# Optimization experiments

Measured on AMD Instinct MI355X. Metric: run time of the kernel, lower is better.

Reference implementation:

```python
import jax, jax.numpy as jnp
import numpy as np
import math

B, S, D, H = 2, 2048, 1024, 16
HD = D // H


def _rms_norm(x, scale):
    # norm over (seq, d_model) jointly per batch element, as in the source
    b, s, d = x.shape
    ff_rms = jnp.sqrt(jnp.sum(x * x, axis=(1, 2))) * (s * d) ** -0.5  # (B,)
    return scale[None, :s, :] * (x / ff_rms[:, None, None])


def _rope(x):
    # faithful to _generate_rope_matrix: theta = 10000^(-2*(i-1)/D) (note i-1)
    b, s, d = x.shape
    i = jnp.arange(d // 2, dtype=jnp.float32)
    theta = 10000.0 ** (-2.0 * (i - 1.0) / d)            # (D/2,)
    ang = jnp.arange(s, dtype=jnp.float32)[:, None] * theta[None, :]  # (S, D/2)
    cos, sin = jnp.cos(ang), jnp.sin(ang)
    xp = x.reshape(b, s, d // 2, 2)
    xe, xo = xp[..., 0], xp[..., 1]
    # out = x @ R[pos]; R block [[cos,-sin],[sin,cos]] per pair
    oe = xe * cos + xo * sin
    oo = -xe * sin + xo * cos
    return jnp.stack([oe, oo], axis=-1).reshape(b, s, d)


def _alibi_mask(s, h):
    r = jnp.arange(s)
    dist = r[:, None] - r[None, :]                        # row j - col i
    base = jnp.where(dist < 0, -jnp.inf, -dist.astype(jnp.float32))  # (S,S)
    ratio = 2.0 ** (-8.0 / h)
    slopes = ratio ** jnp.arange(1, h + 1, dtype=jnp.float32)        # (H,)
    return base[None, :, :] * slopes[:, None, None]       # (H,S,S)


def setup_inputs() -> dict:
    key = jax.random.key(0)
    ks = jax.random.split(key, 9)
    p = lambda k, shp: jax.random.normal(k, shp, jnp.float32) * 0.02
    return {
        "x": jax.random.normal(ks[0], (B, S, D), jnp.float32),
        "Wq": p(ks[1], (D, D)), "Wk": p(ks[2], (D, D)),
        "Wv": p(ks[3], (D, D)), "Wo": p(ks[4], (D, D)),
        "scale1": jnp.ones((S, D), jnp.float32),
        "scale2": jnp.ones((S, D), jnp.float32),
        "W1": p(ks[5], (D, D)), "b1": jnp.zeros((D,), jnp.float32),
        "Wg": p(ks[6], (D, D)), "bg": jnp.zeros((D,), jnp.float32),
        "Wl": p(ks[7], (D, D)), "bl": jnp.zeros((D,), jnp.float32),
        "beta": jnp.ones((1,), jnp.float32),
    }


def reference(x, Wq, Wk, Wv, Wo, scale1, scale2, W1, b1, Wg, bg, Wl, bl, beta):
    b, s, d = x.shape
    # --- attention sublayer ---
    h = _rms_norm(x, scale1)
    q = _rope(h @ Wq)
    k = _rope(h @ Wk)
    v = _rope(h @ Wv)
    qh = q.reshape(b, s, H, HD).transpose(0, 2, 1, 3)  # (B,H,S,HD)
    kh = k.reshape(b, s, H, HD).transpose(0, 2, 1, 3)
    vh = v.reshape(b, s, H, HD).transpose(0, 2, 1, 3)
    mask = _alibi_mask(s, H)                           # (H,S,S)
    scores = jnp.einsum("bhqd,bhkd->bhqk", qh, kh) * (1.0 / math.sqrt(HD))
    probs = jax.nn.softmax(scores + mask[None], axis=-1)
    o = jnp.einsum("bhqk,bhkd->bhqd", probs, vh)
    o = o.transpose(0, 2, 1, 3).reshape(b, s, d)
    x_res_1 = x + o @ Wo
    # --- FFN sublayer: Linear -> SwiGLU ---
    h2 = _rms_norm(x_res_1, scale2) @ W1 + b1
    g = h2 @ Wg + bg
    swish_gate = g * jax.nn.sigmoid(beta * g)
    ffn = swish_gate * (h2 @ Wl + bl)
    return x_res_1 + ffn
```

## Files before the change

### kernel.cpp

```cpp
#include <hip/hip_runtime.h>
#include <hip/hip_bf16.h>

typedef __attribute__((ext_vector_type(8))) short bf16x8;
typedef __attribute__((ext_vector_type(4))) float f32x4;
typedef __attribute__((ext_vector_type(4))) int int4v;

#define DEV static __device__ __forceinline__

DEV float b2f(unsigned short u) { union { unsigned int i; float f; } c; c.i = ((unsigned int)u) << 16; return c.f; }
DEV unsigned short f2b(float f) {
  __hip_bfloat16 h = __float2bfloat16(f);
  unsigned short u; __builtin_memcpy(&u, &h, 2); return u;
}

DEV void gload16(const void* g, void* l) {
  __builtin_amdgcn_global_load_lds(
      (const __attribute__((address_space(1))) unsigned int*)(g),
      (__attribute__((address_space(3))) unsigned int*)(l), 16, 0, 0);
}

__global__ __launch_bounds__(256) void k_transpose_w(const float* __restrict__ W,
                                                     unsigned short* __restrict__ Wt) {
  __shared__ float tile[32][33];
  const int tx = threadIdx.x & 31, ty = threadIdx.x >> 5;
  const int c0 = blockIdx.x * 32, r0 = blockIdx.y * 32;
#pragma unroll
  for (int i = 0; i < 4; ++i)
    tile[ty + i * 8][tx] = W[(size_t)(r0 + ty + i * 8) * 1024 + c0 + tx];
  __syncthreads();
#pragma unroll
  for (int i = 0; i < 4; ++i)
    Wt[(size_t)(c0 + ty + i * 8) * 1024 + r0 + tx] = f2b(tile[tx][ty + i * 8]);
}

__global__ __launch_bounds__(256) void k_reduce_sq(const float* __restrict__ x,
                                                   float* __restrict__ sums) {
  const int b = blockIdx.y;
  const float4* xb = (const float4*)(x + (size_t)b * 2097152);
  float s = 0.f;
  for (int i = blockIdx.x * 256 + threadIdx.x; i < 524288; i += 256 * gridDim.x) {
    float4 v = xb[i];
    s += v.x * v.x + v.y * v.y + v.z * v.z + v.w * v.w;
  }
  __shared__ float red[256];
  red[threadIdx.x] = s;
  __syncthreads();
  for (int st = 128; st > 0; st >>= 1) {
    if (threadIdx.x < st) red[threadIdx.x] += red[threadIdx.x + st];
    __syncthreads();
  }
  if (threadIdx.x == 0) atomicAdd(&sums[b], red[0]);
}

__global__ __launch_bounds__(256) void k_rmsnorm(const float* __restrict__ x,
                                                 const float* __restrict__ scale,
                                                 const float* __restrict__ sums,
                                                 unsigned short* __restrict__ out) {
  const int idx = blockIdx.x * 256 + threadIdx.x;
  const int e = idx * 4;
  const int m = e >> 10, d = e & 1023;
  const int b = m >> 11, s = m & 2047;
  const float inv = rsqrtf(sums[b] * (1.0f / 2097152.0f));
  float4 xv = *(const float4*)(x + (size_t)e);
  float4 sv = *(const float4*)(scale + (size_t)s * 1024 + d);
  ushort4 o;
  o.x = f2b(xv.x * sv.x * inv); o.y = f2b(xv.y * sv.y * inv);
  o.z = f2b(xv.z * sv.z * inv); o.w = f2b(xv.w * sv.w * inv);
  *(ushort4*)(out + e) = o;
}

template <int EPI, int NREP>
__global__ __launch_bounds__(256) void k_gemm(const unsigned short* __restrict__ A,
                                              const unsigned short* __restrict__ Bt,
                                              void* __restrict__ Cout,
                                              const float* __restrict__ aux,
                                              const int N,
                                              float* __restrict__ ss) {
  constexpr int BN = NREP * 32;
  __shared__ short As[128 * 64];
  __shared__ short Bs[BN * 64];
  const int tid = threadIdx.x;
  const int w = tid >> 6, l = tid & 63;
  const int brow = blockIdx.y * 128, bcol = blockIdx.x * BN;
  const int wr = (w >> 1) * 64, wc = (w & 1) * (NREP * 16);
  const int lr = l >> 3, lg = l & 7;
  f32x4 acc[4][NREP] = {};
  const short* Ag = (const short*)A;
  const short* Bg = (const short*)Bt;
  for (int k0 = 0; k0 < 1024; k0 += 64) {
    __syncthreads();
#pragma unroll
    for (int p = 0; p < 4; ++p) {
      const int row = p * 32 + w * 8 + lr;
      gload16(Ag + (size_t)(brow + row) * 1024 + k0 + lg * 8,
              (char*)As + (size_t)(p * 32 + w * 8) * 128);
    }
#pragma unroll
    for (int p = 0; p < NREP; ++p) {
      const int row = p * 32 + w * 8 + lr;
      gload16(Bg + (size_t)(bcol + row) * 1024 + k0 + lg * 8,
              (char*)Bs + (size_t)(p * 32 + w * 8) * 128);
    }
    __syncthreads();
#pragma unroll
    for (int kk = 0; kk < 2; ++kk) {
      const int g0 = kk * 4 + (l >> 4);
      bf16x8 af[4], bfr[NREP];
#pragma unroll
      for (int m = 0; m < 4; ++m)
        af[m] = *(const bf16x8*)(As + (wr + m * 16 + (l & 15)) * 64 + g0 * 8);
#pragma unroll
      for (int n = 0; n < NREP; ++n)
        bfr[n] = *(const bf16x8*)(Bs + (wc + n * 16 + (l & 15)) * 64 + g0 * 8);
#pragma unroll
      for (int m = 0; m < 4; ++m)
#pragma unroll
        for (int n = 0; n < NREP; ++n)
          acc[m][n] = __builtin_amdgcn_mfma_f32_16x16x32_bf16(af[m], bfr[n], acc[m][n], 0, 0, 0);
    }
  }
  const int rr = (l >> 4) * 4, cc = l & 15;
  float sq = 0.f;
#pragma unroll
  for (int m = 0; m < 4; ++m)
#pragma unroll
    for (int n = 0; n < NREP; ++n) {
      const int col = bcol + wc + n * 16 + cc;
#pragma unroll
      for (int j = 0; j < 4; ++j) {
        const int row = brow + wr + m * 16 + rr + j;
        float v = acc[m][n][j];
        if (EPI == 0) {
          ((unsigned short*)Cout)[(size_t)row * N + col] = f2b(v);
        } else if (EPI == 1) {
          const float v2 = aux[(size_t)row * N + col] + v;
          ((float*)Cout)[(size_t)row * N + col] = v2;
          sq += v2 * v2;
        } else {
          ((unsigned short*)Cout)[(size_t)row * N + col] = f2b(v + aux[col]);
        }
      }
    }
  if (EPI == 1) {
#pragma unroll
    for (int off = 1; off < 64; off <<= 1) sq += __shfl_xor(sq, off);
    if (l == 0) atomicAdd(&ss[brow >> 11], sq);
  }
}

__global__ __launch_bounds__(256) void k_rope(unsigned int* __restrict__ qkv32) {
  const int p = blockIdx.x * 256 + threadIdx.x;
  const int m = p / 1536;
  const int pc = p - m * 1536;
  const int s = m & 2047;
  const int i = pc & 511;
  const float theta = expf(-((float)i - 1.0f) * 0.017988946039016f);
  const float ang = (float)s * theta;
  float sn, cs;
  sincosf(ang, &sn, &cs);
  unsigned int v = qkv32[p];
  float xe = b2f((unsigned short)(v & 0xffffu));
  float xo = b2f((unsigned short)(v >> 16));
  float oe = xe * cs + xo * sn;
  float oo = -xe * sn + xo * cs;
  qkv32[p] = (unsigned int)f2b(oe) | ((unsigned int)f2b(oo) << 16);
}

__global__ __launch_bounds__(256) void k_transpose_v(const unsigned short* __restrict__ qkv,
                                                     unsigned short* __restrict__ vt) {
  __shared__ unsigned short tile[32][33];
  const int tx = threadIdx.x & 31, ty = threadIdx.x >> 5;
  const int bh = blockIdx.z;
  const int b = bh >> 4, h = bh & 15;
  const int d0 = blockIdx.x * 32, s0 = blockIdx.y * 32;
#pragma unroll
  for (int i = 0; i < 4; ++i)
    tile[ty + i * 8][tx] = qkv[(size_t)(b * 2048 + s0 + ty + i * 8) * 3072 + 2048 + h * 64 + d0 + tx];
  __syncthreads();
#pragma unroll
  for (int i = 0; i < 4; ++i)
    vt[((size_t)bh * 64 + d0 + ty + i * 8) * 2048 + s0 + tx] = tile[tx][ty + i * 8];
}

__global__ __launch_bounds__(256) void k_attn(const unsigned short* __restrict__ qkv,
                                              const unsigned short* __restrict__ vt,
                                              unsigned short* __restrict__ o) {
  __shared__ short Ks[2][4096];
  __shared__ short Vs[2][4096];
  __shared__ short Ps[4][1280];
  const int h = blockIdx.y, b = blockIdx.z;
  const int qtA = blockIdx.x, qtB = 31 - qtA;
  const int tid = threadIdx.x, w = tid >> 6, l = tid & 63;
  const short* qg = (const short*)qkv;
  bf16x8 aqA0, aqA1, aqB0, aqB1;
  {
    const int rowA = qtA * 64 + w * 16 + (l & 15);
    const short* baseA = qg + (size_t)(b * 2048 + rowA) * 3072 + h * 64 + (l >> 4) * 8;
    aqA0 = *(const bf16x8*)(baseA);
    aqA1 = *(const bf16x8*)(baseA + 32);
    const int rowB = qtB * 64 + w * 16 + (l & 15);
    const short* baseB = qg + (size_t)(b * 2048 + rowB) * 3072 + h * 64 + (l >> 4) * 8;
    aqB0 = *(const bf16x8*)(baseB);
    aqB1 = *(const bf16x8*)(baseB + 32);
  }
  const float slope = exp2f(-0.5f * (float)(h + 1));
  f32x4 oacc[4] = {};
  float mrun[4] = {-1e30f, -1e30f, -1e30f, -1e30f};
  float lrun[4] = {0.f, 0.f, 0.f, 0.f};
  short* Pw = &Ps[w][0];
  const int c0 = tid, c1 = tid + 256;
  const int r0 = c0 >> 3, g0c = c0 & 7;
  const int r1 = c1 >> 3, g1c = c1 & 7;
  const int s0 = r0 * 64 + ((g0c ^ (r0 & 7)) * 8);
  const int s1 = r1 * 64 + ((g1c ^ (r1 & 7)) * 8);
  const short* kbase = qg + (size_t)(b * 2048) * 3072 + 1024 + h * 64;
  const short* vbase = (const short*)vt + (size_t)(b * 16 + h) * 64 * 2048;
  const int nA = qtA + 1;
  const int nt = 33;
  *(int4v*)(&Ks[0][s0]) = *(const int4v*)(kbase + (size_t)r0 * 3072 + g0c * 8);
  *(int4v*)(&Ks[0][s1]) = *(const int4v*)(kbase + (size_t)r1 * 3072 + g1c * 8);
  *(int4v*)(&Vs[0][s0]) = *(const int4v*)(vbase + (size_t)r0 * 2048 + g0c * 8);
  *(int4v*)(&Vs[0][s1]) = *(const int4v*)(vbase + (size_t)r1 * 2048 + g1c * 8);
  __syncthreads();

  auto writeout = [&](int q0w) {
    const int rr = (l >> 4) * 4, cc = l & 15;
#pragma unroll
    for (int n = 0; n < 4; ++n)
#pragma unroll
      for (int j = 0; j < 4; ++j) {
        const int row = q0w + w * 16 + rr + j;
        const int col = h * 64 + n * 16 + cc;
        o[(size_t)(b * 2048 + row) * 1024 + col] = f2b(oacc[n][j] / lrun[j]);
      }
  };

  int cur = 0;
  for (int i = 0; i < nt; ++i) {
    int4v kr0, kr1, vr0, vr1;
    const int inx = i + 1;
    const bool havenext = (inx < nt);
    if (havenext) {
      const int kvn = (inx < nA) ? inx : (inx - nA);
      const size_t k0n = (size_t)kvn * 64;
      kr0 = *(const int4v*)(kbase + (k0n + r0) * 3072 + g0c * 8);
      kr1 = *(const int4v*)(kbase + (k0n + r1) * 3072 + g1c * 8);
      vr0 = *(const int4v*)(vbase + (size_t)r0 * 2048 + k0n + g0c * 8);
      vr1 = *(const int4v*)(vbase + (size_t)r1 * 2048 + k0n + g1c * 8);
    }
    const bool phaseB = (i >= nA);
    const int kvt = phaseB ? (i - nA) : i;
    const int kv0 = kvt * 64;
    const int q0 = (phaseB ? qtB : qtA) * 64;
    const int qw = q0 + w * 16;
    bf16x8 aq0, aq1;
    if (phaseB) { aq0 = aqB0; aq1 = aqB1; } else { aq0 = aqA0; aq1 = aqA1; }
    const short* Ksc = &Ks[cur][0];
    const short* Vsc = &Vs[cur][0];
    f32x4 sacc[4] = {};
    __builtin_amdgcn_s_setprio(1);
#pragma unroll
    for (int kk = 0; kk < 2; ++kk) {
      const int g0r = kk * 4 + (l >> 4);
      const bf16x8 aqk = kk ? aq1 : aq0;
#pragma unroll
      for (int n = 0; n < 4; ++n) {
        const int col = n * 16 + (l & 15);
        bf16x8 bk = *(const bf16x8*)(Ksc + col * 64 + ((g0r ^ (col & 7)) * 8));
        sacc[n] = __builtin_amdgcn_mfma_f32_16x16x32_bf16(aqk, bk, sacc[n], 0, 0, 0);
      }
    }
    __builtin_amdgcn_s_setprio(0);
    float pv[4][4];
    float rm[4] = {-3e30f, -3e30f, -3e30f, -3e30f};
#pragma unroll
    for (int n = 0; n < 4; ++n) {
      const int kvg = kv0 + n * 16 + (l & 15);
#pragma unroll
      for (int j = 0; j < 4; ++j) {
        const int qrow = qw + (l >> 4) * 4 + j;
        float v;
        if (kvg <= qrow) v = sacc[n][j] * 0.125f + slope * (float)(kvg - qrow);
        else v = -1e30f;
        pv[n][j] = v;
        rm[j] = fmaxf(rm[j], v);
      }
    }
#pragma unroll
    for (int j = 0; j < 4; ++j) {
      rm[j] = fmaxf(rm[j], __shfl_xor(rm[j], 1));
      rm[j] = fmaxf(rm[j], __shfl_xor(rm[j], 2));
      rm[j] = fmaxf(rm[j], __shfl_xor(rm[j], 4));
      rm[j] = fmaxf(rm[j], __shfl_xor(rm[j], 8));
    }
    float corr[4], rs[4];
#pragma unroll
    for (int j = 0; j < 4; ++j) {
      const float mn = fmaxf(mrun[j], rm[j]);
      corr[j] = __expf(mrun[j] - mn);
      mrun[j] = mn;
      rs[j] = 0.f;
    }
#pragma unroll
    for (int n = 0; n < 4; ++n)
#pragma unroll
      for (int j = 0; j < 4; ++j) {
        const float e = __expf(pv[n][j] - mrun[j]);
        pv[n][j] = e;
        rs[j] += e;
      }
#pragma unroll
    for (int j = 0; j < 4; ++j) {
      rs[j] += __shfl_xor(rs[j], 1);
      rs[j] += __shfl_xor(rs[j], 2);
      rs[j] += __shfl_xor(rs[j], 4);
      rs[j] += __shfl_xor(rs[j], 8);
      lrun[j] = lrun[j] * corr[j] + rs[j];
    }
#pragma unroll
    for (int n = 0; n < 4; ++n)
#pragma unroll
      for (int j = 0; j < 4; ++j) oacc[n][j] *= corr[j];
#pragma unroll
    for (int n = 0; n < 4; ++n)
#pragma unroll
      for (int j = 0; j < 4; ++j)
        Pw[((l >> 4) * 4 + j) * 80 + n * 16 + (l & 15)] = (short)f2b(pv[n][j]);
    __builtin_amdgcn_s_setprio(1);
#pragma unroll
    for (int kk2 = 0; kk2 < 2; ++kk2) {
      bf16x8 pf = *(const bf16x8*)(Pw + (l & 15) * 80 + kk2 * 32 + (l >> 4) * 8);
#pragma unroll
      for (int n = 0; n < 4; ++n) {
        const int dr = n * 16 + (l & 15);
        bf16x8 vf = *(const bf16x8*)(Vsc + dr * 64 + (((kk2 * 4 + (l >> 4)) ^ (dr & 7)) * 8));
        oacc[n] = __builtin_amdgcn_mfma_f32_16x16x32_bf16(pf, vf, oacc[n], 0, 0, 0);
      }
    }
    __builtin_amdgcn_s_setprio(0);
    if (i == nA - 1) {
      writeout(qtA * 64);
#pragma unroll
      for (int n = 0; n < 4; ++n) oacc[n] = f32x4{0.f, 0.f, 0.f, 0.f};
#pragma unroll
      for (int j = 0; j < 4; ++j) { mrun[j] = -1e30f; lrun[j] = 0.f; }
    }
    if (havenext) {
      const int nxt = cur ^ 1;
      *(int4v*)(&Ks[nxt][s0]) = kr0;
      *(int4v*)(&Ks[nxt][s1]) = kr1;
      *(int4v*)(&Vs[nxt][s0]) = vr0;
      *(int4v*)(&Vs[nxt][s1]) = vr1;
    }
    __syncthreads();
    cur ^= 1;
  }
  writeout(qtB * 64);
}

__global__ __launch_bounds__(256) void k_final(const float* __restrict__ x1,
                                               const unsigned short* __restrict__ gl,
                                               const float* __restrict__ beta,
                                               float* __restrict__ out) {
  const int idx = blockIdx.x * 256 + threadIdx.x;
  const int e = idx * 4;
  const int m = e >> 10, d = e & 1023;
  const float bt = beta[0];
  ushort4 gu = *(const ushort4*)(gl + (size_t)m * 2048 + d);
  ushort4 lu = *(const ushort4*)(gl + (size_t)m * 2048 + 1024 + d);
  float4 xv = *(const float4*)(x1 + e);
  float g0 = b2f(gu.x), g1 = b2f(gu.y), g2 = b2f(gu.z), g3 = b2f(gu.w);
  float l0 = b2f(lu.x), l1 = b2f(lu.y), l2 = b2f(lu.z), l3 = b2f(lu.w);
  float4 r;
  r.x = xv.x + g0 / (1.f + __expf(-bt * g0)) * l0;
  r.y = xv.y + g1 / (1.f + __expf(-bt * g1)) * l1;
  r.z = xv.z + g2 / (1.f + __expf(-bt * g2)) * l2;
  r.w = xv.w + g3 / (1.f + __expf(-bt * g3)) * l3;
  *(float4*)(out + e) = r;
}

extern "C" void kernel_launch(void* const* d_in, const int* in_sizes, int n_in,
                              void* d_out, int out_size, void* d_ws, size_t ws_size,
                              hipStream_t stream) {
  (void)in_sizes; (void)n_in; (void)out_size; (void)ws_size;
  const float* x      = (const float*)d_in[0];
  const float* Wq     = (const float*)d_in[1];
  const float* Wk     = (const float*)d_in[2];
  const float* Wv     = (const float*)d_in[3];
  const float* Wo     = (const float*)d_in[4];
  const float* scale1 = (const float*)d_in[5];
  const float* scale2 = (const float*)d_in[6];
  const float* W1     = (const float*)d_in[7];
  const float* b1     = (const float*)d_in[8];
  const float* Wg     = (const float*)d_in[9];
  const float* bg     = (const float*)d_in[10];
  const float* Wl     = (const float*)d_in[11];
  const float* bl     = (const float*)d_in[12];
  const float* beta   = (const float*)d_in[13];
  float* out = (float*)d_out;

  char* ws = (char*)d_ws;
  float* sums         = (float*)ws;
  float* bgl          = (float*)(ws + 256);
  unsigned short* WT  = (unsigned short*)(ws + 16384);
  unsigned short* h   = (unsigned short*)(ws + 16384 + 6291456);
  unsigned short* qkv = (unsigned short*)((char*)h + 8388608);
  unsigned short* vt  = (unsigned short*)((char*)qkv + 25165824);
  unsigned short* ob  = (unsigned short*)((char*)vt + 8388608);
  float* x1           = (float*)((char*)ob + 8388608);
  unsigned short* t1  = qkv;
  unsigned short* gl  = qkv + 4194304;

  hipMemsetAsync(sums, 0, 256, stream);

  k_transpose_w<<<dim3(32, 32), 256, 0, stream>>>(Wq, WT);
  k_transpose_w<<<dim3(32, 32), 256, 0, stream>>>(Wk, WT + 1048576);
  k_transpose_w<<<dim3(32, 32), 256, 0, stream>>>(Wv, WT + 2097152);
  k_reduce_sq<<<dim3(256, 2), 256, 0, stream>>>(x, sums);
  k_rmsnorm<<<4096, 256, 0, stream>>>(x, scale1, sums, h);
  k_gemm<0, 4><<<dim3(24, 32), 256, 0, stream>>>(h, WT, (void*)qkv, nullptr, 3072, nullptr);
  k_rope<<<24576, 256, 0, stream>>>((unsigned int*)qkv);
  k_transpose_v<<<dim3(2, 64, 32), 256, 0, stream>>>(qkv, vt);
  k_attn<<<dim3(16, 16, 2), 256, 0, stream>>>(qkv, vt, ob);
  k_transpose_w<<<dim3(32, 32), 256, 0, stream>>>(Wo, WT);
  k_gemm<1, 2><<<dim3(16, 32), 256, 0, stream>>>(ob, WT, (void*)x1, x, 1024, sums + 2);

  k_rmsnorm<<<4096, 256, 0, stream>>>(x1, scale2, sums + 2, h);
  k_transpose_w<<<dim3(32, 32), 256, 0, stream>>>(W1, WT);
  k_gemm<2, 2><<<dim3(16, 32), 256, 0, stream>>>(h, WT, (void*)t1, b1, 1024, nullptr);
  k_transpose_w<<<dim3(32, 32), 256, 0, stream>>>(Wg, WT);
  k_transpose_w<<<dim3(32, 32), 256, 0, stream>>>(Wl, WT + 1048576);
  hipMemcpyAsync(bgl, bg, 4096, hipMemcpyDeviceToDevice, stream);
  hipMemcpyAsync(bgl + 1024, bl, 4096, hipMemcpyDeviceToDevice, stream);
  k_gemm<2, 4><<<dim3(16, 32), 256, 0, stream>>>(t1, WT, (void*)gl, bgl, 2048, nullptr);
  k_final<<<4096, 256, 0, stream>>>(x1, gl, beta, out);
}
```

Before: 395.2 us.

## Fuse weight transposes, SwiGLU epilogue, interleave attention tiles, vectorize RoPE

Merges the seven weight-transpose launches into one kernel and drops the bias memcpys. Fuses the SwiGLU, bias and residual into the final GEMM's epilogue, so the gate/linear intermediate and the separate final kernel go away. Restructures attention to process both query tiles of a pair in the same KV loop, computing row sums with an MFMA against a ones vector and using exp2 with folded constants. Remaps attention blocks for XCD locality and vectorizes RoPE with fast sincos, trading some precision for fewer instructions.

```diff
diff --git a/kernel.cpp b/kernel.cpp
--- a/kernel.cpp
+++ b/kernel.cpp
@@ -19,9 +19,22 @@
       (__attribute__((address_space(3))) unsigned int*)(l), 16, 0, 0);
 }
 
-__global__ __launch_bounds__(256) void k_transpose_w(const float* __restrict__ W,
-                                                     unsigned short* __restrict__ Wt) {
+__global__ __launch_bounds__(256) void k_transpose_w7(const float* __restrict__ Wq,
+                                                      const float* __restrict__ Wk,
+                                                      const float* __restrict__ Wv,
+                                                      const float* __restrict__ Wo,
+                                                      const float* __restrict__ W1,
+                                                      const float* __restrict__ Wg,
+                                                      const float* __restrict__ Wl,
+                                                      unsigned short* __restrict__ WT) {
   __shared__ float tile[32][33];
+  const float* W;
+  switch (blockIdx.z) {
+    case 0: W = Wq; break; case 1: W = Wk; break; case 2: W = Wv; break;
+    case 3: W = Wo; break; case 4: W = W1; break; case 5: W = Wg; break;
+    default: W = Wl; break;
+  }
+  unsigned short* dst = WT + (size_t)blockIdx.z * 1048576;
   const int tx = threadIdx.x & 31, ty = threadIdx.x >> 5;
   const int c0 = blockIdx.x * 32, r0 = blockIdx.y * 32;
 #pragma unroll
@@ -30,7 +43,7 @@
   __syncthreads();
 #pragma unroll
   for (int i = 0; i < 4; ++i)
-    Wt[(size_t)(c0 + ty + i * 8) * 1024 + r0 + tx] = f2b(tile[tx][ty + i * 8]);
+    dst[(size_t)(c0 + ty + i * 8) * 1024 + r0 + tx] = f2b(tile[tx][ty + i * 8]);
 }
 
 __global__ __launch_bounds__(256) void k_reduce_sq(const float* __restrict__ x,
@@ -74,6 +87,9 @@
                                               const unsigned short* __restrict__ Bt,
                                               void* __restrict__ Cout,
                                               const float* __restrict__ aux,
+                                              const float* __restrict__ aux2,
+                                              const float* __restrict__ x1p,
+                                              const float* __restrict__ betap,
                                               const int N,
                                               float* __restrict__ ss) {
   constexpr int BN = NREP * 32;
@@ -81,8 +97,10 @@
   __shared__ short Bs[BN * 64];
   const int tid = threadIdx.x;
   const int w = tid >> 6, l = tid & 63;
-  const int brow = blockIdx.y * 128, bcol = blockIdx.x * BN;
-  const int wr = (w >> 1) * 64, wc = (w & 1) * (NREP * 16);
+  const int brow = blockIdx.y * 128;
+  const int bcol = blockIdx.x * (EPI == 4 ? 64 : BN);
+  const int wr = (w >> 1) * 64;
+  const int wc = (EPI == 4) ? (w & 1) * 32 : (w & 1) * (NREP * 16);
   const int lr = l >> 3, lg = l & 7;
   f32x4 acc[4][NREP] = {};
   const short* Ag = (const short*)A;
@@ -98,7 +116,12 @@
 #pragma unroll
     for (int p = 0; p < NREP; ++p) {
       const int row = p * 32 + w * 8 + lr;
-      gload16(Bg + (size_t)(bcol + row) * 1024 + k0 + lg * 8,
+      size_t goff;
+      if (EPI == 4 && p >= 2)
+        goff = (size_t)1048576 + (size_t)(bcol + row - 64) * 1024;
+      else
+        goff = (size_t)(bcol + row) * 1024;
+      gload16(Bg + goff + k0 + lg * 8,
               (char*)Bs + (size_t)(p * 32 + w * 8) * 128);
     }
     __syncthreads();
@@ -110,8 +133,12 @@
       for (int m = 0; m < 4; ++m)
         af[m] = *(const bf16x8*)(As + (wr + m * 16 + (l & 15)) * 64 + g0 * 8);
 #pragma unroll
-      for (int n = 0; n < NREP; ++n)
-        bfr[n] = *(const bf16x8*)(Bs + (wc + n * 16 + (l & 15)) * 64 + g0 * 8);
+      for (int n = 0; n < NREP; ++n) {
+        int bsrow;
+        if (EPI == 4) bsrow = (n < 2) ? (wc + n * 16 + (l & 15)) : (64 + wc + (n - 2) * 16 + (l & 15));
+        else bsrow = wc + n * 16 + (l & 15);
+        bfr[n] = *(const bf16x8*)(Bs + bsrow * 64 + g0 * 8);
+      }
 #pragma unroll
       for (int m = 0; m < 4; ++m)
 #pragma unroll
@@ -120,6 +147,24 @@
     }
   }
   const int rr = (l >> 4) * 4, cc = l & 15;
+  if (EPI == 4) {
+    const float bt = betap[0];
+#pragma unroll
+    for (int m = 0; m < 4; ++m)
+#pragma unroll
+      for (int nn = 0; nn < 2; ++nn) {
+        const int col = bcol + wc + nn * 16 + cc;
+#pragma unroll
+        for (int j = 0; j < 4; ++j) {
+          const int row = brow + wr + m * 16 + rr + j;
+          const float gv = acc[m][nn][j] + aux[col];
+          const float lv = acc[m][nn + 2][j] + aux2[col];
+          const float sw = gv / (1.f + __expf(-bt * gv));
+          ((float*)Cout)[(size_t)row * 1024 + col] = x1p[(size_t)row * 1024 + col] + sw * lv;
+        }
+      }
+    return;
+  }
   float sq = 0.f;
 #pragma unroll
   for (int m = 0; m < 4; ++m)
@@ -149,21 +194,27 @@
 }
 
 __global__ __launch_bounds__(256) void k_rope(unsigned int* __restrict__ qkv32) {
-  const int p = blockIdx.x * 256 + threadIdx.x;
-  const int m = p / 1536;
-  const int pc = p - m * 1536;
+  const int t = blockIdx.x * 256 + threadIdx.x;
+  const int p0 = t * 4;
+  const int m = p0 / 1536;
+  const int pc0 = p0 - m * 1536;
   const int s = m & 2047;
-  const int i = pc & 511;
-  const float theta = expf(-((float)i - 1.0f) * 0.017988946039016f);
-  const float ang = (float)s * theta;
-  float sn, cs;
-  sincosf(ang, &sn, &cs);
-  unsigned int v = qkv32[p];
-  float xe = b2f((unsigned short)(v & 0xffffu));
-  float xo = b2f((unsigned short)(v >> 16));
-  float oe = xe * cs + xo * sn;
-  float oo = -xe * sn + xo * cs;
-  qkv32[p] = (unsigned int)f2b(oe) | ((unsigned int)f2b(oo) << 16);
+  int4v v = *(const int4v*)(qkv32 + p0);
+#pragma unroll
+  for (int z = 0; z < 4; ++z) {
+    const int i = (pc0 + z) & 511;
+    const float theta = exp2f(-((float)i - 1.0f) * 0.0259525627f);
+    const float ang = (float)s * theta;
+    float sn, cs;
+    __sincosf(ang, &sn, &cs);
+    const unsigned int u = (unsigned int)v[z];
+    const float xe = b2f((unsigned short)(u & 0xffffu));
+    const float xo = b2f((unsigned short)(u >> 16));
+    const float oe = xe * cs + xo * sn;
+    const float oo = -xe * sn + xo * cs;
+    v[z] = (int)((unsigned int)f2b(oe) | ((unsigned int)f2b(oo) << 16));
+  }
+  *(int4v*)(qkv32 + p0) = v;
 }
 
 __global__ __launch_bounds__(256) void k_transpose_v(const unsigned short* __restrict__ qkv,
@@ -187,27 +238,37 @@
                                               unsigned short* __restrict__ o) {
   __shared__ short Ks[2][4096];
   __shared__ short Vs[2][4096];
-  __shared__ short Ps[4][1280];
-  const int h = blockIdx.y, b = blockIdx.z;
-  const int qtA = blockIdx.x, qtB = 31 - qtA;
+  __shared__ short Ps[8][1280];
+  const int id = blockIdx.x;
+  const int xcd = id & 7, q = id >> 3;
+  const int p = q & 15, g = (q >> 4) * 8 + xcd;
+  const int h = g & 15, b = g >> 4;
+  const int qtA = p, qtB = 31 - p;
+  const int nA = qtA + 1, nB = qtB + 1;
   const int tid = threadIdx.x, w = tid >> 6, l = tid & 63;
+  const int cc = l & 15, hi = l >> 4;
+  const int qwA = qtA * 64 + w * 16, qwB = qtB * 64 + w * 16;
   const short* qg = (const short*)qkv;
   bf16x8 aqA0, aqA1, aqB0, aqB1;
   {
-    const int rowA = qtA * 64 + w * 16 + (l & 15);
-    const short* baseA = qg + (size_t)(b * 2048 + rowA) * 3072 + h * 64 + (l >> 4) * 8;
-    aqA0 = *(const bf16x8*)(baseA);
+    const short* baseA = qg + (size_t)(b * 2048 + qwA + cc) * 3072 + h * 64 + hi * 8;
+    aqA0 = *(const bf16x8*)baseA;
     aqA1 = *(const bf16x8*)(baseA + 32);
-    const int rowB = qtB * 64 + w * 16 + (l & 15);
-    const short* baseB = qg + (size_t)(b * 2048 + rowB) * 3072 + h * 64 + (l >> 4) * 8;
-    aqB0 = *(const bf16x8*)(baseB);
+    const short* baseB = qg + (size_t)(b * 2048 + qwB + cc) * 3072 + h * 64 + hi * 8;
+    aqB0 = *(const bf16x8*)baseB;
     aqB1 = *(const bf16x8*)(baseB + 32);
   }
-  const float slope = exp2f(-0.5f * (float)(h + 1));
-  f32x4 oacc[4] = {};
-  float mrun[4] = {-1e30f, -1e30f, -1e30f, -1e30f};
-  float lrun[4] = {0.f, 0.f, 0.f, 0.f};
-  short* Pw = &Ps[w][0];
+  const float slope2 = exp2f(-0.5f * (float)(h + 1)) * 1.44269504f;
+  const float C1 = 0.125f * 1.44269504f;
+  bf16x8 onesf;
+#pragma unroll
+  for (int z = 0; z < 8; ++z) onesf[z] = (short)0x3F80;
+  f32x4 oaccA[4] = {}, oaccB[4] = {};
+  f32x4 rsA = {}, rsB = {};
+  float mA[4] = {-1e30f, -1e30f, -1e30f, -1e30f};
+  float mB[4] = {-1e30f, -1e30f, -1e30f, -1e30f};
+  short* PwA = &Ps[w][0];
+  short* PwB = &Ps[w + 4][0];
   const int c0 = tid, c1 = tid + 256;
   const int r0 = c0 >> 3, g0c = c0 & 7;
   const int r1 = c1 >> 3, g1c = c1 & 7;
@@ -215,136 +276,118 @@
   const int s1 = r1 * 64 + ((g1c ^ (r1 & 7)) * 8);
   const short* kbase = qg + (size_t)(b * 2048) * 3072 + 1024 + h * 64;
   const short* vbase = (const short*)vt + (size_t)(b * 16 + h) * 64 * 2048;
-  const int nA = qtA + 1;
-  const int nt = 33;
   *(int4v*)(&Ks[0][s0]) = *(const int4v*)(kbase + (size_t)r0 * 3072 + g0c * 8);
   *(int4v*)(&Ks[0][s1]) = *(const int4v*)(kbase + (size_t)r1 * 3072 + g1c * 8);
   *(int4v*)(&Vs[0][s0]) = *(const int4v*)(vbase + (size_t)r0 * 2048 + g0c * 8);
   *(int4v*)(&Vs[0][s1]) = *(const int4v*)(vbase + (size_t)r1 * 2048 + g1c * 8);
   __syncthreads();
 
-  auto writeout = [&](int q0w) {
-    const int rr = (l >> 4) * 4, cc = l & 15;
+  auto sm_pv = [&](f32x4 (&sacc)[4], f32x4 (&oacc)[4], f32x4& rs, float (&mr)[4],
+                   short* Pw, const int qw, const bool domask, const int kv0,
+                   const short* Vsc) {
+    float alib[4];
+#pragma unroll
+    for (int n = 0; n < 4; ++n) alib[n] = slope2 * (float)(kv0 + n * 16 + cc);
+    float sc[4][4], rm4[4];
+#pragma unroll
+    for (int j = 0; j < 4; ++j) rm4[j] = -3e30f;
 #pragma unroll
     for (int n = 0; n < 4; ++n)
 #pragma unroll
       for (int j = 0; j < 4; ++j) {
-        const int row = q0w + w * 16 + rr + j;
-        const int col = h * 64 + n * 16 + cc;
-        o[(size_t)(b * 2048 + row) * 1024 + col] = f2b(oacc[n][j] / lrun[j]);
-      }
+        float v = fmaf(sacc[n][j], C1, alib[n]);
+        if (domask) {
+          const int kvg = kv0 + n * 16 + cc;
+          const int qrow = qw + hi * 4 + j;
+          v = (kvg <= qrow) ? v : -1e30f;
+        }
+        sc[n][j] = v;
+        rm4[j] = fmaxf(rm4[j], v);
+      }
+#pragma unroll
+    for (int j = 0; j < 4; ++j) {
+      rm4[j] = fmaxf(rm4[j], __shfl_xor(rm4[j], 1));
+      rm4[j] = fmaxf(rm4[j], __shfl_xor(rm4[j], 2));
+      rm4[j] = fmaxf(rm4[j], __shfl_xor(rm4[j], 4));
+      rm4[j] = fmaxf(rm4[j], __shfl_xor(rm4[j], 8));
+    }
+    float corr[4];
+#pragma unroll
+    for (int j = 0; j < 4; ++j) {
+      const float mn = fmaxf(mr[j], rm4[j]);
+      corr[j] = exp2f(mr[j] - mn);
+      mr[j] = mn;
+    }
+#pragma unroll
+    for (int n = 0; n < 4; ++n)
+#pragma unroll
+      for (int j = 0; j < 4; ++j)
+        Pw[(hi * 4 + j) * 80 + n * 16 + cc] = (short)f2b(exp2f(sc[n][j] - mr[j]));
+#pragma unroll
+    for (int n = 0; n < 4; ++n)
+#pragma unroll
+      for (int j = 0; j < 4; ++j) oacc[n][j] *= corr[j];
+#pragma unroll
+    for (int j = 0; j < 4; ++j) rs[j] *= corr[j];
+    __builtin_amdgcn_s_setprio(1);
+#pragma unroll
+    for (int kk2 = 0; kk2 < 2; ++kk2) {
+      bf16x8 pf = *(const bf16x8*)(Pw + cc * 80 + kk2 * 32 + hi * 8);
+      rs = __builtin_amdgcn_mfma_f32_16x16x32_bf16(pf, onesf, rs, 0, 0, 0);
+#pragma unroll
+      for (int n = 0; n < 4; ++n) {
+        const int dr = n * 16 + cc;
+        bf16x8 vf = *(const bf16x8*)(Vsc + dr * 64 + (((kk2 * 4 + hi) ^ (dr & 7)) * 8));
+        oacc[n] = __builtin_amdgcn_mfma_f32_16x16x32_bf16(pf, vf, oacc[n], 0, 0, 0);
+      }
+    }
+    __builtin_amdgcn_s_setprio(0);
   };
 
   int cur = 0;
-  for (int i = 0; i < nt; ++i) {
+  for (int t = 0; t < nB; ++t) {
     int4v kr0, kr1, vr0, vr1;
-    const int inx = i + 1;
-    const bool havenext = (inx < nt);
+    const bool havenext = (t + 1 < nB);
     if (havenext) {
-      const int kvn = (inx < nA) ? inx : (inx - nA);
-      const size_t k0n = (size_t)kvn * 64;
+      const size_t k0n = (size_t)(t + 1) * 64;
       kr0 = *(const int4v*)(kbase + (k0n + r0) * 3072 + g0c * 8);
       kr1 = *(const int4v*)(kbase + (k0n + r1) * 3072 + g1c * 8);
       vr0 = *(const int4v*)(vbase + (size_t)r0 * 2048 + k0n + g0c * 8);
       vr1 = *(const int4v*)(vbase + (size_t)r1 * 2048 + k0n + g1c * 8);
     }
-    const bool phaseB = (i >= nA);
-    const int kvt = phaseB ? (i - nA) : i;
-    const int kv0 = kvt * 64;
-    const int q0 = (phaseB ? qtB : qtA) * 64;
-    const int qw = q0 + w * 16;
-    bf16x8 aq0, aq1;
-    if (phaseB) { aq0 = aqB0; aq1 = aqB1; } else { aq0 = aqA0; aq1 = aqA1; }
+    const int kv0 = t * 64;
     const short* Ksc = &Ks[cur][0];
     const short* Vsc = &Vs[cur][0];
-    f32x4 sacc[4] = {};
+    const bool doA = (t < nA);
+    f32x4 sB[4] = {}, sA[4] = {};
     __builtin_amdgcn_s_setprio(1);
 #pragma unroll
     for (int kk = 0; kk < 2; ++kk) {
-      const int g0r = kk * 4 + (l >> 4);
-      const bf16x8 aqk = kk ? aq1 : aq0;
+      const int g0r = kk * 4 + hi;
+      const bf16x8 aqk = kk ? aqB1 : aqB0;
 #pragma unroll
       for (int n = 0; n < 4; ++n) {
-        const int col = n * 16 + (l & 15);
+        const int col = n * 16 + cc;
         bf16x8 bk = *(const bf16x8*)(Ksc + col * 64 + ((g0r ^ (col & 7)) * 8));
-        sacc[n] = __builtin_amdgcn_mfma_f32_16x16x32_bf16(aqk, bk, sacc[n], 0, 0, 0);
+        sB[n] = __builtin_amdgcn_mfma_f32_16x16x32_bf16(aqk, bk, sB[n], 0, 0, 0);
+      }
+    }
+    if (doA) {
+#pragma unroll
+      for (int kk = 0; kk < 2; ++kk) {
+        const int g0r = kk * 4 + hi;
+        const bf16x8 aqk = kk ? aqA1 : aqA0;
+#pragma unroll
+        for (int n = 0; n < 4; ++n) {
+          const int col = n * 16 + cc;
+          bf16x8 bk = *(const bf16x8*)(Ksc + col * 64 + ((g0r ^ (col & 7)) * 8));
+          sA[n] = __builtin_amdgcn_mfma_f32_16x16x32_bf16(aqk, bk, sA[n], 0, 0, 0);
+        }
       }
     }
     __builtin_amdgcn_s_setprio(0);
-    float pv[4][4];
-    float rm[4] = {-3e30f, -3e30f, -3e30f, -3e30f};
-#pragma unroll
-    for (int n = 0; n < 4; ++n) {
-      const int kvg = kv0 + n * 16 + (l & 15);
-#pragma unroll
-      for (int j = 0; j < 4; ++j) {
-        const int qrow = qw + (l >> 4) * 4 + j;
-        float v;
-        if (kvg <= qrow) v = sacc[n][j] * 0.125f + slope * (float)(kvg - qrow);
-        else v = -1e30f;
-        pv[n][j] = v;
-        rm[j] = fmaxf(rm[j], v);
-      }
-    }
-#pragma unroll
-    for (int j = 0; j < 4; ++j) {
-      rm[j] = fmaxf(rm[j], __shfl_xor(rm[j], 1));
-      rm[j] = fmaxf(rm[j], __shfl_xor(rm[j], 2));
-      rm[j] = fmaxf(rm[j], __shfl_xor(rm[j], 4));
-      rm[j] = fmaxf(rm[j], __shfl_xor(rm[j], 8));
-    }
-    float corr[4], rs[4];
-#pragma unroll
-    for (int j = 0; j < 4; ++j) {
-      const float mn = fmaxf(mrun[j], rm[j]);
-      corr[j] = __expf(mrun[j] - mn);
-      mrun[j] = mn;
-      rs[j] = 0.f;
-    }
-#pragma unroll
-    for (int n = 0; n < 4; ++n)
-#pragma unroll
-      for (int j = 0; j < 4; ++j) {
-        const float e = __expf(pv[n][j] - mrun[j]);
-        pv[n][j] = e;
-        rs[j] += e;
-      }
-#pragma unroll
-    for (int j = 0; j < 4; ++j) {
-      rs[j] += __shfl_xor(rs[j], 1);
-      rs[j] += __shfl_xor(rs[j], 2);
-      rs[j] += __shfl_xor(rs[j], 4);
-      rs[j] += __shfl_xor(rs[j], 8);
-      lrun[j] = lrun[j] * corr[j] + rs[j];
-    }
-#pragma unroll
-    for (int n = 0; n < 4; ++n)
-#pragma unroll
-      for (int j = 0; j < 4; ++j) oacc[n][j] *= corr[j];
-#pragma unroll
-    for (int n = 0; n < 4; ++n)
-#pragma unroll
-      for (int j = 0; j < 4; ++j)
-        Pw[((l >> 4) * 4 + j) * 80 + n * 16 + (l & 15)] = (short)f2b(pv[n][j]);
-    __builtin_amdgcn_s_setprio(1);
-#pragma unroll
-    for (int kk2 = 0; kk2 < 2; ++kk2) {
-      bf16x8 pf = *(const bf16x8*)(Pw + (l & 15) * 80 + kk2 * 32 + (l >> 4) * 8);
-#pragma unroll
-      for (int n = 0; n < 4; ++n) {
-        const int dr = n * 16 + (l & 15);
-        bf16x8 vf = *(const bf16x8*)(Vsc + dr * 64 + (((kk2 * 4 + (l >> 4)) ^ (dr & 7)) * 8));
-        oacc[n] = __builtin_amdgcn_mfma_f32_16x16x32_bf16(pf, vf, oacc[n], 0, 0, 0);
-      }
-    }
-    __builtin_amdgcn_s_setprio(0);
-    if (i == nA - 1) {
-      writeout(qtA * 64);
-#pragma unroll
-      for (int n = 0; n < 4; ++n) oacc[n] = f32x4{0.f, 0.f, 0.f, 0.f};
-#pragma unroll
-      for (int j = 0; j < 4; ++j) { mrun[j] = -1e30f; lrun[j] = 0.f; }
-    }
+    sm_pv(sB, oaccB, rsB, mB, PwB, qwB, t == nB - 1, kv0, Vsc);
+    if (doA) sm_pv(sA, oaccA, rsA, mA, PwA, qwA, t == nA - 1, kv0, Vsc);
     if (havenext) {
       const int nxt = cur ^ 1;
       *(int4v*)(&Ks[nxt][s0]) = kr0;
@@ -355,28 +398,23 @@
     __syncthreads();
     cur ^= 1;
   }
-  writeout(qtB * 64);
-}
-
-__global__ __launch_bounds__(256) void k_final(const float* __restrict__ x1,
-                                               const unsigned short* __restrict__ gl,
-                                               const float* __restrict__ beta,
-                                               float* __restrict__ out) {
-  const int idx = blockIdx.x * 256 + threadIdx.x;
-  const int e = idx * 4;
-  const int m = e >> 10, d = e & 1023;
-  const float bt = beta[0];
-  ushort4 gu = *(const ushort4*)(gl + (size_t)m * 2048 + d);
-  ushort4 lu = *(const ushort4*)(gl + (size_t)m * 2048 + 1024 + d);
-  float4 xv = *(const float4*)(x1 + e);
-  float g0 = b2f(gu.x), g1 = b2f(gu.y), g2 = b2f(gu.z), g3 = b2f(gu.w);
-  float l0 = b2f(lu.x), l1 = b2f(lu.y), l2 = b2f(lu.z), l3 = b2f(lu.w);
-  float4 r;
-  r.x = xv.x + g0 / (1.f + __expf(-bt * g0)) * l0;
-  r.y = xv.y + g1 / (1.f + __expf(-bt * g1)) * l1;
-  r.z = xv.z + g2 / (1.f + __expf(-bt * g2)) * l2;
-  r.w = xv.w + g3 / (1.f + __expf(-bt * g3)) * l3;
-  *(float4*)(out + e) = r;
+  {
+    const int rr = hi * 4;
+#pragma unroll
+    for (int n = 0; n < 4; ++n)
+#pragma unroll
+      for (int j = 0; j < 4; ++j) {
+        const int row = qwA + rr + j;
+        o[(size_t)(b * 2048 + row) * 1024 + h * 64 + n * 16 + cc] = f2b(oaccA[n][j] / rsA[j]);
+      }
+#pragma unroll
+    for (int n = 0; n < 4; ++n)
+#pragma unroll
+      for (int j = 0; j < 4; ++j) {
+        const int row = qwB + rr + j;
+        o[(size_t)(b * 2048 + row) * 1024 + h * 64 + n * 16 + cc] = f2b(oaccB[n][j] / rsB[j]);
+      }
+  }
 }
 
 extern "C" void kernel_launch(void* const* d_in, const int* in_sizes, int n_in,
@@ -401,37 +439,26 @@
 
   char* ws = (char*)d_ws;
   float* sums         = (float*)ws;
-  float* bgl          = (float*)(ws + 256);
   unsigned short* WT  = (unsigned short*)(ws + 16384);
-  unsigned short* h   = (unsigned short*)(ws + 16384 + 6291456);
+  unsigned short* h   = (unsigned short*)(ws + 16384 + 14680064);
   unsigned short* qkv = (unsigned short*)((char*)h + 8388608);
   unsigned short* vt  = (unsigned short*)((char*)qkv + 25165824);
-  unsigned short* ob  = (unsigned short*)((char*)vt + 8388608);
-  float* x1           = (float*)((char*)ob + 8388608);
+  float* x1           = (float*)((char*)vt + 8388608);
+  unsigned short* ob  = h;
   unsigned short* t1  = qkv;
-  unsigned short* gl  = qkv + 4194304;
 
   hipMemsetAsync(sums, 0, 256, stream);
 
-  k_transpose_w<<<dim3(32, 32), 256, 0, stream>>>(Wq, WT);
-  k_transpose_w<<<dim3(32, 32), 256, 0, stream>>>(Wk, WT + 1048576);
-  k_transpose_w<<<dim3(32, 32), 256, 0, stream>>>(Wv, WT + 2097152);
+  k_transpose_w7<<<dim3(32, 32, 7), 256, 0, stream>>>(Wq, Wk, Wv, Wo, W1, Wg, Wl, WT);
   k_reduce_sq<<<dim3(256, 2), 256, 0, stream>>>(x, sums);
   k_rmsnorm<<<4096, 256, 0, stream>>>(x, scale1, sums, h);
-  k_gemm<0, 4><<<dim3(24, 32), 256, 0, stream>>>(h, WT, (void*)qkv, nullptr, 3072, nullptr);
-  k_rope<<<24576, 256, 0, stream>>>((unsigned int*)qkv);
+  k_gemm<0, 4><<<dim3(24, 32), 256, 0, stream>>>(h, WT, (void*)qkv, nullptr, nullptr, nullptr, nullptr, 3072, nullptr);
+  k_rope<<<6144, 256, 0, stream>>>((unsigned int*)qkv);
   k_transpose_v<<<dim3(2, 64, 32), 256, 0, stream>>>(qkv, vt);
-  k_attn<<<dim3(16, 16, 2), 256, 0, stream>>>(qkv, vt, ob);
-  k_transpose_w<<<dim3(32, 32), 256, 0, stream>>>(Wo, WT);
-  k_gemm<1, 2><<<dim3(16, 32), 256, 0, stream>>>(ob, WT, (void*)x1, x, 1024, sums + 2);
+  k_attn<<<512, 256, 0, stream>>>(qkv, vt, ob);
+  k_gemm<1, 2><<<dim3(16, 32), 256, 0, stream>>>(ob, WT + 3145728, (void*)x1, x, nullptr, nullptr, nullptr, 1024, sums + 2);
 
   k_rmsnorm<<<4096, 256, 0, stream>>>(x1, scale2, sums + 2, h);
-  k_transpose_w<<<dim3(32, 32), 256, 0, stream>>>(W1, WT);
-  k_gemm<2, 2><<<dim3(16, 32), 256, 0, stream>>>(h, WT, (void*)t1, b1, 1024, nullptr);
-  k_transpose_w<<<dim3(32, 32), 256, 0, stream>>>(Wg, WT);
-  k_transpose_w<<<dim3(32, 32), 256, 0, stream>>>(Wl, WT + 1048576);
-  hipMemcpyAsync(bgl, bg, 4096, hipMemcpyDeviceToDevice, stream);
-  hipMemcpyAsync(bgl + 1024, bl, 4096, hipMemcpyDeviceToDevice, stream);
-  k_gemm<2, 4><<<dim3(16, 32), 256, 0, stream>>>(t1, WT, (void*)gl, bgl, 2048, nullptr);
-  k_final<<<4096, 256, 0, stream>>>(x1, gl, beta, out);
-}
+  k_gemm<2, 2><<<dim3(16, 32), 256, 0, stream>>>(h, WT + 4194304, (void*)t1, b1, nullptr, nullptr, nullptr, 1024, nullptr);
+  k_gemm<4, 4><<<dim3(16, 32), 256, 0, stream>>>(t1, WT + 5242880, (void*)out, bg, bl, x1, beta, 1024, nullptr);
+}
```

After: 367.8 us. 6.9% less time.
